# Kernel optimization log

Measured on AMD Instinct MI355X. Metric: run time of the kernel, lower is better.

Reference implementation:

```python
import jax, jax.numpy as jnp
import numpy as np

NP, NA = 60000, 30000          # paper / author node counts
EC, EW, EB = 300000, 150000, 150000
IN_F, HID, H, D, NCLS = 1024, 512, 4, 128, 153  # HID = H*D


def setup_inputs() -> dict:
    key = jax.random.key(0)
    ks = jax.random.split(key, 24)
    inp = {
        "x_paper": jax.random.normal(ks[0], (NP, IN_F), jnp.float32),
        "x_author": jax.random.normal(ks[1], (NA, IN_F), jnp.float32),
        "cites_src": jax.random.randint(ks[2], (EC,), 0, NP, jnp.int32),
        "cites_dst": jax.random.randint(ks[3], (EC,), 0, NP, jnp.int32),
        "writes_src": jax.random.randint(ks[4], (EW,), 0, NA, jnp.int32),
        "writes_dst": jax.random.randint(ks[5], (EW,), 0, NP, jnp.int32),
        "wb_src": jax.random.randint(ks[6], (EB,), 0, NP, jnp.int32),
        "wb_dst": jax.random.randint(ks[7], (EB,), 0, NA, jnp.int32),
        "W0": jax.random.normal(ks[8], (3, IN_F, HID), jnp.float32) * 0.02,
        "al0": jax.random.normal(ks[9], (3, H, D), jnp.float32) * 0.1,
        "ar0": jax.random.normal(ks[10], (3, H, D), jnp.float32) * 0.1,
        "W1": jax.random.normal(ks[11], (3, HID, HID), jnp.float32) * 0.03,
        "al1": jax.random.normal(ks[12], (3, H, D), jnp.float32) * 0.1,
        "ar1": jax.random.normal(ks[13], (3, H, D), jnp.float32) * 0.1,
        "W2": jax.random.normal(ks[14], (3, HID, HID), jnp.float32) * 0.03,
        "al2": jax.random.normal(ks[15], (3, H, D), jnp.float32) * 0.1,
        "ar2": jax.random.normal(ks[16], (3, H, D), jnp.float32) * 0.1,
        "linW": jax.random.normal(ks[17], (HID, NCLS), jnp.float32) * 0.02,
        "linb": jnp.zeros((NCLS,), jnp.float32),
    }
    return inp


def gat_conv(h_src, h_dst, src, dst, W, al, ar, n_dst):
    """DGL-style GATConv on one edge type (bipartite block, shared fc)."""
    zs = (h_src @ W).reshape(-1, H, D)            # (Ns,H,D)
    zd = (h_dst @ W).reshape(-1, H, D)            # (Nd,H,D)
    el = jnp.sum(zs * al, axis=-1)                # (Ns,H)
    er = jnp.sum(zd * ar, axis=-1)                # (Nd,H)
    e = jax.nn.leaky_relu(el[src] + er[dst], 0.2)  # (E,H)
    # edge softmax over incoming edges per destination node
    m = jax.ops.segment_max(e, dst, num_segments=n_dst)
    m = jnp.where(jnp.isfinite(m), m, 0.0)
    ee = jnp.exp(e - m[dst])
    s = jax.ops.segment_sum(ee, dst, num_segments=n_dst)
    a = ee / (s[dst] + 1e-9)                      # (E,H)
    # weighted message aggregation: (Nd,H,D)
    return jax.ops.segment_sum(a[:, :, None] * zs[src], dst, num_segments=n_dst)


def reference(x_paper, x_author, cites_src, cites_dst, writes_src, writes_dst,
              wb_src, wb_dst, W0, al0, ar0, W1, al1, ar1, W2, al2, ar2,
              linW, linb):
    def hetero_layer(hp, ha, W, al, ar, act):
        # HeteroGraphConv: sum-aggregate per destination node type
        op = (gat_conv(hp, hp, cites_src, cites_dst, W[0], al[0], ar[0], NP)
              + gat_conv(ha, hp, writes_src, writes_dst, W[1], al[1], ar[1], NP))
        oa = gat_conv(hp, ha, wb_src, wb_dst, W[2], al[2], ar[2], NA)
        op = op.reshape(NP, H * D)   # head-flatten as in forward()
        oa = oa.reshape(NA, H * D)
        if act:
            op, oa = jax.nn.relu(op), jax.nn.relu(oa)
        return op, oa

    hp, ha = x_paper, x_author
    hp, ha = hetero_layer(hp, ha, W0, al0, ar0, True)
    hp, ha = hetero_layer(hp, ha, W1, al1, ar1, True)
    hp, ha = hetero_layer(hp, ha, W2, al2, ar2, False)  # last layer: no activation
    return hp @ linW + linb
```

## Files before the change

kernel.cpp:

```cpp
#include <hip/hip_runtime.h>
#include <cstddef>
#include <cstdint>

static constexpr int NP = 60000, NA = 30000;
static constexpr int EC = 300000, EW = 150000, EB = 150000;
static constexpr int IN_F = 1024, HID = 512, H = 4, D = 128, NCLS = 153;
static constexpr int MPAD_P = 60160;
static constexpr int MPAD_A = 30208;

typedef __attribute__((ext_vector_type(8))) short short8;
typedef __attribute__((ext_vector_type(4))) float float4v;

__device__ __forceinline__ unsigned short f2bf(float f) {
    unsigned int u = __float_as_uint(f);
    unsigned int r = u + 0x7FFFu + ((u >> 16) & 1u);
    return (unsigned short)(r >> 16);
}
__device__ __forceinline__ float bf2f(unsigned short h) {
    return __uint_as_float(((unsigned int)h) << 16);
}

__device__ __forceinline__ void gll16(const unsigned short* g, unsigned short* l) {
    __builtin_amdgcn_global_load_lds(
        (const __attribute__((address_space(1))) unsigned int*)g,
        (__attribute__((address_space(3))) unsigned int*)l, 16, 0, 0);
}

__global__ void hist_kernel(const int* __restrict__ dst, int E, int* __restrict__ counts) {
    int e = blockIdx.x * 256 + threadIdx.x;
    if (e < E) atomicAdd(&counts[dst[e]], 1);
}

__global__ void exscan_kernel(const int* __restrict__ in, int* __restrict__ out, int n) {
    __shared__ int wsum[4];
    int t = threadIdx.x;
    int lane = t & 63, w = t >> 6;
    int carry = 0;
    const int CH = 256 * 8;
    for (int base = 0; base < n; base += CH) {
        int v[8], run[8];
        int i0 = base + t * 8;
        int tsum = 0;
#pragma unroll
        for (int j = 0; j < 8; ++j) {
            int i = i0 + j;
            v[j] = (i < n) ? in[i] : 0;
            tsum += v[j];
            run[j] = tsum;
        }
        int x = tsum;
#pragma unroll
        for (int off = 1; off < 64; off <<= 1) {
            int y = __shfl_up(x, off);
            if (lane >= off) x += y;
        }
        if (lane == 63) wsum[w] = x;
        __syncthreads();
        int wpre = 0;
        for (int ww = 0; ww < w; ++ww) wpre += wsum[ww];
        int chunktot = wsum[0] + wsum[1] + wsum[2] + wsum[3];
        int pre = carry + wpre + (x - tsum);
#pragma unroll
        for (int j = 0; j < 8; ++j) {
            int i = i0 + j;
            if (i < n) out[i] = pre + run[j] - v[j];
        }
        carry += chunktot;
        __syncthreads();
    }
    if (t == 0) out[n] = carry;
}

__global__ void fill_kernel(const int* __restrict__ src, const int* __restrict__ dst, int E,
                            int* __restrict__ cursor, int* __restrict__ col) {
    int e = blockIdx.x * 256 + threadIdx.x;
    if (e < E) {
        int pos = atomicAdd(&cursor[dst[e]], 1);
        col[pos] = src[e];
    }
}

__global__ void decomp4_kernel(const float4* __restrict__ x, ushort4* __restrict__ hi,
                               ushort4* __restrict__ lo, int M, int K, int Mpad) {
    size_t i4 = (size_t)blockIdx.x * 256 + threadIdx.x;
    size_t tot = ((size_t)Mpad * K) >> 2;
    if (i4 >= tot) return;
    size_t row = (i4 * 4) / (size_t)K;
    float4 v = make_float4(0.f, 0.f, 0.f, 0.f);
    if (row < (size_t)M) v = x[i4];
    ushort4 h, l;
    h.x = f2bf(v.x); h.y = f2bf(v.y); h.z = f2bf(v.z); h.w = f2bf(v.w);
    l.x = f2bf(v.x - bf2f(h.x)); l.y = f2bf(v.y - bf2f(h.y));
    l.z = f2bf(v.z - bf2f(h.z)); l.w = f2bf(v.w - bf2f(h.w));
    hi[i4] = h; lo[i4] = l;
}

__global__ void btprep_kernel(const float* __restrict__ W, unsigned short* __restrict__ hi,
                              unsigned short* __restrict__ lo, int K, int N, int Npad) {
    int i = blockIdx.x * 256 + threadIdx.x;
    if (i >= Npad * K) return;
    int n = i / K, k = i - n * K;
    float v = (n < N) ? W[(size_t)k * N + n] : 0.f;
    unsigned short h = f2bf(v);
    hi[i] = h;
    lo[i] = f2bf(v - bf2f(h));
}

__global__ __launch_bounds__(512, 2) void gemm_6ph(
    const unsigned short* __restrict__ Ahi, const unsigned short* __restrict__ Alo,
    const unsigned short* __restrict__ Bhi, const unsigned short* __restrict__ Blo,
    const float* __restrict__ bias, float* __restrict__ C,
    int M, int K, int Nstore, int ldc) {
    extern __shared__ unsigned short lds[];
    const int tid = threadIdx.x;
    const int lane = tid & 63;
    const int w = tid >> 6;
    const int wr = w >> 2, wc = w & 3;
    const int bm = blockIdx.y * 256, bn = blockIdx.x * 256;

    const int st_row = w * 16 + (lane >> 2);
    const int st_sc = (((lane & 3) ^ ((lane >> 3) & 3)) << 3);
    const size_t aoff0 = (size_t)(bm + st_row) * K + st_sc;
    const size_t aoff1 = aoff0 + (size_t)128 * K;
    const size_t boff0 = (size_t)(bn + st_row) * K + st_sc;
    const size_t boff1 = boff0 + (size_t)128 * K;
    const int ldsAo = w * 512;
    const int ldsBo = 8192 + w * 512;

    const int arow = wr * 128 + (lane & 15);
    const int brow = wc * 64 + (lane & 15);
    const int rq = ((((lane >> 4) & 3) ^ ((lane >> 1) & 3)) << 3);
    const int aRead = arow * 32 + rq;
    const int bRead = 8192 + brow * 32 + rq;

    float4v acc[8][4];
    float4v zf = {0.f, 0.f, 0.f, 0.f};
#pragma unroll
    for (int i = 0; i < 8; ++i)
#pragma unroll
        for (int j = 0; j < 4; ++j) acc[i][j] = zf;

#define WAITV(n) asm volatile("s_waitcnt vmcnt(" #n ")" ::: "memory")
#define BARF()                                 \
    do {                                       \
        asm volatile("" ::: "memory");         \
        __builtin_amdgcn_s_barrier();          \
        asm volatile("" ::: "memory");         \
    } while (0)
#define PRIO1 __builtin_amdgcn_s_setprio(1)
#define PRIO0 __builtin_amdgcn_s_setprio(0)
#define MF(a, b, c) __builtin_amdgcn_mfma_f32_16x16x32_bf16(a, b, c, 0, 0, 0)

#define CHUNK(RG, DOSTAGE, KN, W2STMT, W6STMT)                                        \
    do {                                                                              \
        const unsigned short* sA = &lds[(RG) * 16384u];             \
        const unsigned short* sB = &lds[((RG) + 1u) * 16384u];      \
        unsigned short* dA = &lds[((RG) ^ 2u) * 16384u];                              \
        unsigned short* dB = &lds[(((RG) ^ 2u) + 1u) * 16384u];                       \
        short8 fahi[8], falo[8], fbhi[4], fblo[4];                                    \
                                                                  \
        _Pragma("unroll") for (int i = 0; i < 4; ++i)                                 \
            fahi[i] = *(const short8*)&sA[aRead + i * 512];                           \
        _Pragma("unroll") for (int j = 0; j < 4; ++j)                                 \
            fbhi[j] = *(const short8*)&sA[bRead + j * 512];                           \
        if (DOSTAGE) {                                                                \
            gll16(Ahi + aoff0 + (KN), dA + ldsAo);                                    \
            gll16(Ahi + aoff1 + (KN), dA + ldsAo + 4096);                             \
        }                                                                             \
        BARF(); PRIO1;                                                                \
        _Pragma("unroll") for (int i = 0; i < 4; ++i)                                 \
            _Pragma("unroll") for (int j = 0; j < 4; ++j)                             \
                acc[i][j] = MF(fahi[i], fbhi[j], acc[i][j]);                          \
        PRIO0; BARF();                                                                \
                                                                  \
        _Pragma("unroll") for (int i = 0; i < 4; ++i)                                 \
            fahi[i + 4] = *(const short8*)&sA[aRead + (i + 4) * 512];                 \
        if (DOSTAGE) {                                                                \
            gll16(Bhi + boff0 + (KN), dA + ldsBo);                                    \
            gll16(Bhi + boff1 + (KN), dA + ldsBo + 4096);                             \
        }                                                                             \
        BARF(); PRIO1;                                                                \
        _Pragma("unroll") for (int i = 0; i < 4; ++i)                                 \
            _Pragma("unroll") for (int j = 0; j < 4; ++j)                             \
                acc[i + 4][j] = MF(fahi[i + 4], fbhi[j], acc[i + 4][j]);              \
        PRIO0; W2STMT; BARF();                                                        \
                                                                  \
        _Pragma("unroll") for (int i = 0; i < 4; ++i)                                 \
            falo[i] = *(const short8*)&sB[aRead + i * 512];                           \
        if (DOSTAGE) {                                                                \
            gll16(Alo + aoff0 + (KN), dB + ldsAo);                                    \
            gll16(Alo + aoff1 + (KN), dB + ldsAo + 4096);                             \
        }                                                                             \
        BARF(); PRIO1;                                                                \
        _Pragma("unroll") for (int i = 0; i < 4; ++i)                                 \
            _Pragma("unroll") for (int j = 0; j < 4; ++j)                             \
                acc[i][j] = MF(falo[i], fbhi[j], acc[i][j]);                          \
        PRIO0; BARF();                                                                \
                                                                  \
        _Pragma("unroll") for (int i = 0; i < 4; ++i)                                 \
            falo[i + 4] = *(const short8*)&sB[aRead + (i + 4) * 512];                 \
        if (DOSTAGE) {                                                                \
            gll16(Blo + boff0 + (KN), dB + ldsBo);                                    \
            gll16(Blo + boff1 + (KN), dB + ldsBo + 4096);                             \
        }                                                                             \
        BARF(); PRIO1;                                                                \
        _Pragma("unroll") for (int i = 0; i < 4; ++i)                                 \
            _Pragma("unroll") for (int j = 0; j < 4; ++j)                             \
                acc[i + 4][j] = MF(falo[i + 4], fbhi[j], acc[i + 4][j]);              \
        PRIO0; BARF();                                                                \
                                      \
        _Pragma("unroll") for (int j = 0; j < 4; ++j)                                 \
            fblo[j] = *(const short8*)&sB[bRead + j * 512];                           \
        BARF(); PRIO1;                                                                \
        _Pragma("unroll") for (int i = 0; i < 8; ++i)                                 \
            _Pragma("unroll") for (int j = 0; j < 4; ++j)                             \
                acc[i][j] = MF(fahi[i], fblo[j], acc[i][j]);                          \
        PRIO0; W6STMT; BARF();                                                        \
    } while (0)

    gll16(Ahi + aoff0, &lds[0] + ldsAo);
    gll16(Ahi + aoff1, &lds[0] + ldsAo + 4096);
    gll16(Bhi + boff0, &lds[0] + ldsBo);
    gll16(Bhi + boff1, &lds[0] + ldsBo + 4096);
    gll16(Alo + aoff0, &lds[16384] + ldsAo);
    gll16(Alo + aoff1, &lds[16384] + ldsAo + 4096);
    gll16(Blo + boff0, &lds[16384] + ldsBo);
    gll16(Blo + boff1, &lds[16384] + ldsBo + 4096);
    WAITV(4);
    BARF();

    unsigned rg = 0;
    const int nK = K >> 5;
#pragma unroll 1
    for (int c = 0; c < nK - 1; ++c) {
        const int kn = (c + 1) << 5;
        CHUNK(rg, 1, kn, WAITV(4), WAITV(4));
        rg ^= 2;
    }
    CHUNK(rg, 0, 0, WAITV(0), (void)0);
#undef CHUNK
#undef MF
#undef PRIO1
#undef PRIO0
#undef WAITV
#undef BARF

    const int col0 = bn + wc * 64 + (lane & 15);
    const int row0 = bm + wr * 128 + ((lane >> 4) << 2);
#pragma unroll
    for (int i = 0; i < 8; ++i) {
#pragma unroll
        for (int j = 0; j < 4; ++j) {
            int col = col0 + j * 16;
            if (col >= Nstore) continue;
            float badd = bias ? bias[col] : 0.f;
            int rowb = row0 + i * 16;
#pragma unroll
            for (int k = 0; k < 4; ++k) {
                int row = rowb + k;
                if (row < M) C[(size_t)row * ldc + col] = acc[i][j][k] + badd;
            }
        }
    }
}

__global__ __launch_bounds__(256) void eler_kernel(
    const float* __restrict__ z, const float* __restrict__ al, const float* __restrict__ ar,
    float* __restrict__ el, float* __restrict__ er, int M) {
    int row = blockIdx.x * 4 + (threadIdx.x >> 6);
    int lane = threadIdx.x & 63;
    if (row >= M) return;
    const float4* zr = (const float4*)(z + (size_t)row * 512 + lane * 8);
    float4 z0 = zr[0], z1 = zr[1];
    const float4* alp = (const float4*)(al + lane * 8);
    float4 a0 = alp[0], a1 = alp[1];
    float s = z0.x * a0.x + z0.y * a0.y + z0.z * a0.z + z0.w * a0.w
            + z1.x * a1.x + z1.y * a1.y + z1.z * a1.z + z1.w * a1.w;
    s += __shfl_xor(s, 8); s += __shfl_xor(s, 4); s += __shfl_xor(s, 2); s += __shfl_xor(s, 1);
    int h = lane >> 4;
    if ((lane & 15) == 0) el[(size_t)row * 4 + h] = s;
    if (er) {
        const float4* arp = (const float4*)(ar + lane * 8);
        float4 b0 = arp[0], b1 = arp[1];
        float t = z0.x * b0.x + z0.y * b0.y + z0.z * b0.z + z0.w * b0.w
                + z1.x * b1.x + z1.y * b1.y + z1.z * b1.z + z1.w * b1.w;
        t += __shfl_xor(t, 8); t += __shfl_xor(t, 4); t += __shfl_xor(t, 2); t += __shfl_xor(t, 1);
        if ((lane & 15) == 0) er[(size_t)row * 4 + h] = t;
    }
}

__global__ void fold_kernel(const float* __restrict__ W, const float* __restrict__ ar,
                            float* __restrict__ v, int K) {
    int i = blockIdx.x * 256 + threadIdx.x;
    if (i >= K * 4) return;
    int k = i >> 2, h = i & 3;
    const float* wr = W + (size_t)k * 512 + h * 128;
    const float* a = ar + h * 128;
    float s = 0.f;
#pragma unroll 4
    for (int d = 0; d < 128; ++d) s += wr[d] * a[d];
    v[i] = s;
}

__global__ __launch_bounds__(256) void skinny_kernel(
    const float* __restrict__ h, const float* __restrict__ v,
    float* __restrict__ er, int M, int K) {
    __shared__ float vs[4096];
    for (int i = threadIdx.x; i < K * 4; i += 256) vs[i] = v[i];
    __syncthreads();
    int row = blockIdx.x * 4 + (threadIdx.x >> 6);
    int lane = threadIdx.x & 63;
    if (row >= M) return;
    const float* hr = h + (size_t)row * K;
    float a0 = 0, a1 = 0, a2 = 0, a3 = 0;
    for (int k = lane; k < K; k += 64) {
        float x = hr[k];
        float4 vv = *(const float4*)&vs[k * 4];
        a0 += x * vv.x; a1 += x * vv.y; a2 += x * vv.z; a3 += x * vv.w;
    }
#pragma unroll
    for (int off = 32; off; off >>= 1) {
        a0 += __shfl_xor(a0, off); a1 += __shfl_xor(a1, off);
        a2 += __shfl_xor(a2, off); a3 += __shfl_xor(a3, off);
    }
    if (lane == 0) *(float4*)&er[(size_t)row * 4] = make_float4(a0, a1, a2, a3);
}

__global__ __launch_bounds__(256) void agg_fused(
    const int* __restrict__ rp1, const int* __restrict__ col1, const float* __restrict__ z1,
    const float* __restrict__ el1, const float* __restrict__ er1,
    const int* __restrict__ rp2, const int* __restrict__ col2, const float* __restrict__ z2,
    const float* __restrict__ el2, const float* __restrict__ er2,
    float* __restrict__ out, unsigned short* __restrict__ hi, unsigned short* __restrict__ lo,
    int N, int do_relu) {
    int j = blockIdx.x * 4 + (threadIdx.x >> 6);
    int lane = threadIdx.x & 63;
    if (j >= N) return;
    int h = lane >> 4;
    float4 acc0 = make_float4(0, 0, 0, 0), acc1 = make_float4(0, 0, 0, 0);

    {
        int e0 = rp1[j], e1 = rp1[j + 1];
        float erh = er1[(size_t)j * 4 + h];
        float m = -INFINITY, s = 0.f;
        for (int e = e0; e < e1; ++e) {
            float x = el1[(size_t)col1[e] * 4 + h] + erh;
            x = (x >= 0.f) ? x : 0.2f * x;
            float mn = fmaxf(m, x);
            s = s * expf(m - mn) + expf(x - mn);
            m = mn;
        }
        float inv = 1.0f / (s + 1e-9f);
        for (int e = e0; e < e1; ++e) {
            int src = col1[e];
            float x = el1[(size_t)src * 4 + h] + erh;
            x = (x >= 0.f) ? x : 0.2f * x;
            float wgt = expf(x - m) * inv;
            const float4* zr = (const float4*)(z1 + (size_t)src * 512 + lane * 8);
            float4 za = zr[0], zb = zr[1];
            acc0.x += wgt * za.x; acc0.y += wgt * za.y; acc0.z += wgt * za.z; acc0.w += wgt * za.w;
            acc1.x += wgt * zb.x; acc1.y += wgt * zb.y; acc1.z += wgt * zb.z; acc1.w += wgt * zb.w;
        }
    }
    if (rp2) {
        int e0 = rp2[j], e1 = rp2[j + 1];
        float erh = er2[(size_t)j * 4 + h];
        float m = -INFINITY, s = 0.f;
        for (int e = e0; e < e1; ++e) {
            float x = el2[(size_t)col2[e] * 4 + h] + erh;
            x = (x >= 0.f) ? x : 0.2f * x;
            float mn = fmaxf(m, x);
            s = s * expf(m - mn) + expf(x - mn);
            m = mn;
        }
        float inv = 1.0f / (s + 1e-9f);
        for (int e = e0; e < e1; ++e) {
            int src = col2[e];
            float x = el2[(size_t)src * 4 + h] + erh;
            x = (x >= 0.f) ? x : 0.2f * x;
            float wgt = expf(x - m) * inv;
            const float4* zr = (const float4*)(z2 + (size_t)src * 512 + lane * 8);
            float4 za = zr[0], zb = zr[1];
            acc0.x += wgt * za.x; acc0.y += wgt * za.y; acc0.z += wgt * za.z; acc0.w += wgt * za.w;
            acc1.x += wgt * zb.x; acc1.y += wgt * zb.y; acc1.z += wgt * zb.z; acc1.w += wgt * zb.w;
        }
    }
    if (do_relu) {
        acc0.x = fmaxf(acc0.x, 0.f); acc0.y = fmaxf(acc0.y, 0.f);
        acc0.z = fmaxf(acc0.z, 0.f); acc0.w = fmaxf(acc0.w, 0.f);
        acc1.x = fmaxf(acc1.x, 0.f); acc1.y = fmaxf(acc1.y, 0.f);
        acc1.z = fmaxf(acc1.z, 0.f); acc1.w = fmaxf(acc1.w, 0.f);
    }
    float* op = out + (size_t)j * 512 + lane * 8;
    *(float4*)op = acc0;
    *(float4*)(op + 4) = acc1;
    if (hi) {
        size_t base = (size_t)j * 512 + lane * 8;
        ushort4 h0, h1, l0, l1;
        h0.x = f2bf(acc0.x); h0.y = f2bf(acc0.y); h0.z = f2bf(acc0.z); h0.w = f2bf(acc0.w);
        h1.x = f2bf(acc1.x); h1.y = f2bf(acc1.y); h1.z = f2bf(acc1.z); h1.w = f2bf(acc1.w);
        l0.x = f2bf(acc0.x - bf2f(h0.x)); l0.y = f2bf(acc0.y - bf2f(h0.y));
        l0.z = f2bf(acc0.z - bf2f(h0.z)); l0.w = f2bf(acc0.w - bf2f(h0.w));
        l1.x = f2bf(acc1.x - bf2f(h1.x)); l1.y = f2bf(acc1.y - bf2f(h1.y));
        l1.z = f2bf(acc1.z - bf2f(h1.z)); l1.w = f2bf(acc1.w - bf2f(h1.w));
        *(ushort4*)(hi + base) = h0;
        *(ushort4*)(hi + base + 4) = h1;
        *(ushort4*)(lo + base) = l0;
        *(ushort4*)(lo + base + 4) = l1;
    }
}

extern "C" void kernel_launch(void* const* d_in, const int* in_sizes, int n_in,
                              void* d_out, int out_size, void* d_ws, size_t ws_size,
                              hipStream_t stream) {
    const float* x_paper = (const float*)d_in[0];
    const float* x_author = (const float*)d_in[1];
    const int* cites_src = (const int*)d_in[2];
    const int* cites_dst = (const int*)d_in[3];
    const int* writes_src = (const int*)d_in[4];
    const int* writes_dst = (const int*)d_in[5];
    const int* wb_src = (const int*)d_in[6];
    const int* wb_dst = (const int*)d_in[7];
    const float* W0 = (const float*)d_in[8];
    const float* al0 = (const float*)d_in[9];
    const float* ar0 = (const float*)d_in[10];
    const float* W1 = (const float*)d_in[11];
    const float* al1 = (const float*)d_in[12];
    const float* ar1 = (const float*)d_in[13];
    const float* W2 = (const float*)d_in[14];
    const float* al2 = (const float*)d_in[15];
    const float* ar2 = (const float*)d_in[16];
    const float* linW = (const float*)d_in[17];
    const float* linb = (const float*)d_in[18];
    float* out = (float*)d_out;

    (void)hipFuncSetAttribute((const void*)gemm_6ph,
                              hipFuncAttributeMaxDynamicSharedMemorySize, 131072);

    char* p = (char*)d_ws;
    auto alloc = [&](size_t n) { char* r = p; p += (n + 255) & ~(size_t)255; return r; };

    float* hpA = (float*)alloc((size_t)NP * 512 * 4);
    float* hpB = (float*)alloc((size_t)NP * 512 * 4);
    float* haA = (float*)alloc((size_t)NA * 512 * 4);
    float* haB = (float*)alloc((size_t)NA * 512 * 4);
    float* zbuf = (float*)alloc((size_t)NP * 512 * 4);
    float* elA = (float*)alloc((size_t)NP * 16);
    float* erA = (float*)alloc((size_t)NP * 16);
    float* elB = (float*)alloc((size_t)NP * 16);
    float* erB = (float*)alloc((size_t)NP * 16);
    float* vfold = (float*)alloc(4096 * 4);
    int* rp_c = (int*)alloc((NP + 1) * 4);
    int* col_c = (int*)alloc((size_t)EC * 4);
    int* rp_w = (int*)alloc((NP + 1) * 4);
    int* col_w = (int*)alloc((size_t)EW * 4);
    int* rp_b = (int*)alloc((NA + 1) * 4);
    int* col_b = (int*)alloc((size_t)EB * 4);
    int* cursor = (int*)alloc((NP + 1) * 4);
    int* counts = (int*)alloc((size_t)NP * 4);

    unsigned short* AhiP = (unsigned short*)alloc((size_t)MPAD_P * 1024 * 2);
    unsigned short* AloP = (unsigned short*)alloc((size_t)MPAD_P * 1024 * 2);
    unsigned short* AhiA = (unsigned short*)alloc((size_t)MPAD_A * 1024 * 2);
    unsigned short* AloA = (unsigned short*)alloc((size_t)MPAD_A * 1024 * 2);
    const int Ks[3] = {IN_F, HID, HID};
    unsigned short *bthi[3][3], *btlo[3][3];
    for (int l = 0; l < 3; ++l)
        for (int t = 0; t < 3; ++t) {
            bthi[l][t] = (unsigned short*)alloc((size_t)512 * Ks[l] * 2);
            btlo[l][t] = (unsigned short*)alloc((size_t)512 * Ks[l] * 2);
        }
    unsigned short* btLhi = (unsigned short*)alloc((size_t)256 * 512 * 2);
    unsigned short* btLlo = (unsigned short*)alloc((size_t)256 * 512 * 2);
    (void)ws_size;

    struct EdgeT { const int* src; const int* dst; int E; int n; int* rp; int* col; };
    EdgeT ets[3] = {
        {cites_src, cites_dst, EC, NP, rp_c, col_c},
        {writes_src, writes_dst, EW, NP, rp_w, col_w},
        {wb_src, wb_dst, EB, NA, rp_b, col_b},
    };
    for (int t = 0; t < 3; ++t) {
        hipMemsetAsync(counts, 0, (size_t)ets[t].n * 4, stream);
        hist_kernel<<<(ets[t].E + 255) / 256, 256, 0, stream>>>(ets[t].dst, ets[t].E, counts);
        exscan_kernel<<<1, 256, 0, stream>>>(counts, ets[t].rp, ets[t].n);
        hipMemcpyAsync(cursor, ets[t].rp, (size_t)ets[t].n * 4, hipMemcpyDeviceToDevice, stream);
        fill_kernel<<<(ets[t].E + 255) / 256, 256, 0, stream>>>(ets[t].src, ets[t].dst, ets[t].E, cursor, ets[t].col);
    }

    const float* Wl[3] = {W0, W1, W2};
    const float* alL[3] = {al0, al1, al2};
    const float* arL[3] = {ar0, ar1, ar2};

    for (int l = 0; l < 3; ++l) {
        int K = Ks[l];
        for (int t = 0; t < 3; ++t)
            btprep_kernel<<<(512 * K + 255) / 256, 256, 0, stream>>>(
                Wl[l] + (size_t)t * K * 512, bthi[l][t], btlo[l][t], K, 512, 512);
    }
    btprep_kernel<<<(256 * 512 + 255) / 256, 256, 0, stream>>>(linW, btLhi, btLlo, 512, NCLS, 256);

    decomp4_kernel<<<((size_t)MPAD_P * 1024 / 4 + 255) / 256, 256, 0, stream>>>(
        (const float4*)x_paper, (ushort4*)AhiP, (ushort4*)AloP, NP, 1024, MPAD_P);
    decomp4_kernel<<<((size_t)MPAD_A * 1024 / 4 + 255) / 256, 256, 0, stream>>>(
        (const float4*)x_author, (ushort4*)AhiA, (ushort4*)AloA, NA, 1024, MPAD_A);

    auto gemm = [&](const unsigned short* Ah, const unsigned short* Al,
                    const unsigned short* Bh, const unsigned short* Bl,
                    const float* bias, float* C, int M, int Mpad, int K, int gx,
                    int Nstore, int ldc) {
        dim3 g(gx, Mpad / 256);
        gemm_6ph<<<g, 512, 131072, stream>>>(Ah, Al, Bh, Bl, bias, C, M, K, Nstore, ldc);
    };

    const float* hp = x_paper;
    const float* ha = x_author;
    for (int l = 0; l < 3; ++l) {
        int K = Ks[l];
        float* hp_n = (l & 1) ? hpB : hpA;
        float* ha_n = (l & 1) ? haB : haA;
        float* zbuf_w = ha_n;
        const float* W = Wl[l];
        const float* al = alL[l];
        const float* ar = arL[l];
        size_t wstride = (size_t)K * 512;
        int relu = (l < 2) ? 1 : 0;

        gemm(AhiP, AloP, bthi[l][0], btlo[l][0], nullptr, zbuf, NP, MPAD_P, K, 2, 512, 512);
        gemm(AhiA, AloA, bthi[l][1], btlo[l][1], nullptr, zbuf_w, NA, MPAD_A, K, 2, 512, 512);
        eler_kernel<<<(NP + 3) / 4, 256, 0, stream>>>(zbuf, al, ar, elA, erA, NP);
        eler_kernel<<<(NA + 3) / 4, 256, 0, stream>>>(zbuf_w, al + 512, nullptr, elB, nullptr, NA);
        fold_kernel<<<(K * 4 + 255) / 256, 256, 0, stream>>>(W + wstride, ar + 512, vfold, K);
        skinny_kernel<<<(NP + 3) / 4, 256, 0, stream>>>(hp, vfold, erB, NP, K);
        agg_fused<<<(NP + 3) / 4, 256, 0, stream>>>(
            rp_c, col_c, zbuf, elA, erA,
            rp_w, col_w, zbuf_w, elB, erB,
            hp_n, nullptr, nullptr, NP, relu);
        gemm(AhiP, AloP, bthi[l][2], btlo[l][2], nullptr, zbuf, NP, MPAD_P, K, 2, 512, 512);
        decomp4_kernel<<<((size_t)MPAD_P * 512 / 4 + 255) / 256, 256, 0, stream>>>(
            (const float4*)hp_n, (ushort4*)AhiP, (ushort4*)AloP, NP, 512, MPAD_P);
        eler_kernel<<<(NP + 3) / 4, 256, 0, stream>>>(zbuf, al + 1024, nullptr, elA, nullptr, NP);
        fold_kernel<<<(K * 4 + 255) / 256, 256, 0, stream>>>(W + 2 * wstride, ar + 1024, vfold, K);
        skinny_kernel<<<(NA + 3) / 4, 256, 0, stream>>>(ha, vfold, erA, NA, K);
        agg_fused<<<(NA + 3) / 4, 256, 0, stream>>>(
            rp_b, col_b, zbuf, elA, erA,
            nullptr, nullptr, nullptr, nullptr, nullptr,
            ha_n, (l < 2) ? AhiA : nullptr, (l < 2) ? AloA : nullptr, NA, relu);
        hp = hp_n;
        ha = ha_n;
    }
    gemm(AhiP, AloP, btLhi, btLlo, linb, out, NP, MPAD_P, 512, 1, NCLS, NCLS);
}
```

Measured before the change: 3.216 ms.

## Restructure split-bf16 GEMM chunk into register-prefetched five-phase pipeline

```diff
diff --git a/kernel.cpp b/kernel.cpp
--- a/kernel.cpp
+++ b/kernel.cpp
@@ -106,7 +106,7 @@
     lo[i] = f2bf(v - bf2f(h));
 }
 
-__global__ __launch_bounds__(512, 2) void gemm_6ph(
+__global__ __launch_bounds__(512, 2) void gemm_ra(
     const unsigned short* __restrict__ Ahi, const unsigned short* __restrict__ Alo,
     const unsigned short* __restrict__ Bhi, const unsigned short* __restrict__ Blo,
     const float* __restrict__ bias, float* __restrict__ C,
@@ -140,82 +140,93 @@
 #pragma unroll
         for (int j = 0; j < 4; ++j) acc[i][j] = zf;
 
-#define WAITV(n) asm volatile("s_waitcnt vmcnt(" #n ")" ::: "memory")
-#define BARF()                                 \
-    do {                                       \
-        asm volatile("" ::: "memory");         \
-        __builtin_amdgcn_s_barrier();          \
-        asm volatile("" ::: "memory");         \
+    short8 faL[4], fbL[4], faU[4], flL[4], flU[4], fblo[4], nxA[4], nxB[4];
+
+#define SBAR() __builtin_amdgcn_sched_barrier(0)
+#define WAITV(n)                                      \
+    do {                                              \
+        asm volatile("s_waitcnt vmcnt(" #n ")");      \
+        SBAR();                                       \
+    } while (0)
+#define BAR()                                         \
+    do {                                              \
+        SBAR();                                       \
+        __builtin_amdgcn_s_barrier();                 \
+        SBAR();                                       \
     } while (0)
 #define PRIO1 __builtin_amdgcn_s_setprio(1)
 #define PRIO0 __builtin_amdgcn_s_setprio(0)
 #define MF(a, b, c) __builtin_amdgcn_mfma_f32_16x16x32_bf16(a, b, c, 0, 0, 0)
 
-#define CHUNK(RG, DOSTAGE, KN, W2STMT, W6STMT)                                        \
+#define CHUNK(RG, DOSTAGE, KN, W1STMT, W3STMT, W4STMT, LASTC)                         \
     do {                                                                              \
         const unsigned short* sA = &lds[(RG) * 16384u];             \
         const unsigned short* sB = &lds[((RG) + 1u) * 16384u];      \
         unsigned short* dA = &lds[((RG) ^ 2u) * 16384u];                              \
         unsigned short* dB = &lds[(((RG) ^ 2u) + 1u) * 16384u];                       \
-        short8 fahi[8], falo[8], fbhi[4], fblo[4];                                    \
-                                                                  \
-        _Pragma("unroll") for (int i = 0; i < 4; ++i)                                 \
-            fahi[i] = *(const short8*)&sA[aRead + i * 512];                           \
-        _Pragma("unroll") for (int j = 0; j < 4; ++j)                                 \
-            fbhi[j] = *(const short8*)&sA[bRead + j * 512];                           \
+                            \
+        _Pragma("unroll") for (int i = 0; i < 4; ++i)                                 \
+            faU[i] = *(const short8*)&sA[aRead + (i + 4) * 512];                      \
         if (DOSTAGE) {                                                                \
             gll16(Ahi + aoff0 + (KN), dA + ldsAo);                                    \
             gll16(Ahi + aoff1 + (KN), dA + ldsAo + 4096);                             \
         }                                                                             \
-        BARF(); PRIO1;                                                                \
-        _Pragma("unroll") for (int i = 0; i < 4; ++i)                                 \
-            _Pragma("unroll") for (int j = 0; j < 4; ++j)                             \
-                acc[i][j] = MF(fahi[i], fbhi[j], acc[i][j]);                          \
-        PRIO0; BARF();                                                                \
-                                                                  \
-        _Pragma("unroll") for (int i = 0; i < 4; ++i)                                 \
-            fahi[i + 4] = *(const short8*)&sA[aRead + (i + 4) * 512];                 \
+        PRIO1;                                                                        \
+        _Pragma("unroll") for (int i = 0; i < 4; ++i)                                 \
+            _Pragma("unroll") for (int j = 0; j < 4; ++j)                             \
+                acc[i][j] = MF(faL[i], fbL[j], acc[i][j]);                            \
+        PRIO0; W1STMT; BAR();                                                         \
+                                  \
+        _Pragma("unroll") for (int i = 0; i < 4; ++i)                                 \
+            flL[i] = *(const short8*)&sB[aRead + i * 512];                            \
         if (DOSTAGE) {                                                                \
             gll16(Bhi + boff0 + (KN), dA + ldsBo);                                    \
             gll16(Bhi + boff1 + (KN), dA + ldsBo + 4096);                             \
         }                                                                             \
-        BARF(); PRIO1;                                                                \
-        _Pragma("unroll") for (int i = 0; i < 4; ++i)                                 \
-            _Pragma("unroll") for (int j = 0; j < 4; ++j)                             \
-                acc[i + 4][j] = MF(fahi[i + 4], fbhi[j], acc[i + 4][j]);              \
-        PRIO0; W2STMT; BARF();                                                        \
-                                                                  \
-        _Pragma("unroll") for (int i = 0; i < 4; ++i)                                 \
-            falo[i] = *(const short8*)&sB[aRead + i * 512];                           \
+        PRIO1;                                                                        \
+        _Pragma("unroll") for (int i = 0; i < 4; ++i)                                 \
+            _Pragma("unroll") for (int j = 0; j < 4; ++j)                             \
+                acc[i + 4][j] = MF(faU[i], fbL[j], acc[i + 4][j]);                    \
+        PRIO0; BAR();                                                                 \
+                                 \
+        _Pragma("unroll") for (int i = 0; i < 4; ++i)                                 \
+            flU[i] = *(const short8*)&sB[aRead + (i + 4) * 512];                      \
         if (DOSTAGE) {                                                                \
             gll16(Alo + aoff0 + (KN), dB + ldsAo);                                    \
             gll16(Alo + aoff1 + (KN), dB + ldsAo + 4096);                             \
         }                                                                             \
-        BARF(); PRIO1;                                                                \
-        _Pragma("unroll") for (int i = 0; i < 4; ++i)                                 \
-            _Pragma("unroll") for (int j = 0; j < 4; ++j)                             \
-                acc[i][j] = MF(falo[i], fbhi[j], acc[i][j]);                          \
-        PRIO0; BARF();                                                                \
-                                                                  \
-        _Pragma("unroll") for (int i = 0; i < 4; ++i)                                 \
-            falo[i + 4] = *(const short8*)&sB[aRead + (i + 4) * 512];                 \
+        PRIO1;                                                                        \
+        _Pragma("unroll") for (int i = 0; i < 4; ++i)                                 \
+            _Pragma("unroll") for (int j = 0; j < 4; ++j)                             \
+                acc[i][j] = MF(flL[i], fbL[j], acc[i][j]);                            \
+        PRIO0; W3STMT; BAR();                                                         \
+                                 \
+        _Pragma("unroll") for (int j = 0; j < 4; ++j)                                 \
+            fblo[j] = *(const short8*)&sB[bRead + j * 512];                           \
         if (DOSTAGE) {                                                                \
             gll16(Blo + boff0 + (KN), dB + ldsBo);                                    \
             gll16(Blo + boff1 + (KN), dB + ldsBo + 4096);                             \
         }                                                                             \
-        BARF(); PRIO1;                                                                \
-        _Pragma("unroll") for (int i = 0; i < 4; ++i)                                 \
-            _Pragma("unroll") for (int j = 0; j < 4; ++j)                             \
-                acc[i + 4][j] = MF(falo[i + 4], fbhi[j], acc[i + 4][j]);              \
-        PRIO0; BARF();                                                                \
-                                      \
-        _Pragma("unroll") for (int j = 0; j < 4; ++j)                                 \
-            fblo[j] = *(const short8*)&sB[bRead + j * 512];                           \
-        BARF(); PRIO1;                                                                \
-        _Pragma("unroll") for (int i = 0; i < 8; ++i)                                 \
-            _Pragma("unroll") for (int j = 0; j < 4; ++j)                             \
-                acc[i][j] = MF(fahi[i], fblo[j], acc[i][j]);                          \
-        PRIO0; W6STMT; BARF();                                                        \
+        PRIO1;                                                                        \
+        _Pragma("unroll") for (int i = 0; i < 4; ++i)                                 \
+            _Pragma("unroll") for (int j = 0; j < 4; ++j)                             \
+                acc[i + 4][j] = MF(flU[i], fbL[j], acc[i + 4][j]);                    \
+        PRIO0; W4STMT; BAR();                                                         \
+             \
+        if (!(LASTC)) {                                                               \
+            _Pragma("unroll") for (int i = 0; i < 4; ++i)                             \
+                nxA[i] = *(const short8*)&dA[aRead + i * 512];                        \
+            _Pragma("unroll") for (int j = 0; j < 4; ++j)                             \
+                nxB[j] = *(const short8*)&dA[bRead + j * 512];                        \
+        }                                                                             \
+        PRIO1;                                                                        \
+        _Pragma("unroll") for (int i = 0; i < 4; ++i)                                 \
+            _Pragma("unroll") for (int j = 0; j < 4; ++j)                             \
+                acc[i][j] = MF(faL[i], fblo[j], acc[i][j]);                           \
+        _Pragma("unroll") for (int i = 0; i < 4; ++i)                                 \
+            _Pragma("unroll") for (int j = 0; j < 4; ++j)                             \
+                acc[i + 4][j] = MF(faU[i], fblo[j], acc[i + 4][j]);                   \
+        PRIO0; BAR();                                                                 \
     } while (0)
 
     gll16(Ahi + aoff0, &lds[0] + ldsAo);
@@ -227,23 +238,30 @@
     gll16(Blo + boff0, &lds[16384] + ldsBo);
     gll16(Blo + boff1, &lds[16384] + ldsBo + 4096);
     WAITV(4);
-    BARF();
+    BAR();
+#pragma unroll
+    for (int i = 0; i < 4; ++i) faL[i] = *(const short8*)&lds[aRead + i * 512];
+#pragma unroll
+    for (int j = 0; j < 4; ++j) fbL[j] = *(const short8*)&lds[bRead + j * 512];
 
     unsigned rg = 0;
     const int nK = K >> 5;
 #pragma unroll 1
     for (int c = 0; c < nK - 1; ++c) {
         const int kn = (c + 1) << 5;
-        CHUNK(rg, 1, kn, WAITV(4), WAITV(4));
+        CHUNK(rg, 1, kn, WAITV(4), WAITV(6), WAITV(4), 0);
+#pragma unroll
+        for (int i = 0; i < 4; ++i) { faL[i] = nxA[i]; fbL[i] = nxB[i]; }
         rg ^= 2;
     }
-    CHUNK(rg, 0, 0, WAITV(0), (void)0);
+    CHUNK(rg, 0, 0, WAITV(2), WAITV(0), (void)0, 1);
 #undef CHUNK
 #undef MF
 #undef PRIO1
 #undef PRIO0
+#undef BAR
 #undef WAITV
-#undef BARF
+#undef SBAR
 
     const int col0 = bn + wc * 64 + (lane & 15);
     const int row0 = bm + wr * 128 + ((lane >> 4) << 2);
@@ -434,7 +452,7 @@
     const float* linb = (const float*)d_in[18];
     float* out = (float*)d_out;
 
-    (void)hipFuncSetAttribute((const void*)gemm_6ph,
+    (void)hipFuncSetAttribute((const void*)gemm_ra,
                               hipFuncAttributeMaxDynamicSharedMemorySize, 131072);
 
     char* p = (char*)d_ws;
@@ -510,7 +528,7 @@
                     const float* bias, float* C, int M, int Mpad, int K, int gx,
                     int Nstore, int ldc) {
         dim3 g(gx, Mpad / 256);
-        gemm_6ph<<<g, 512, 131072, stream>>>(Ah, Al, Bh, Bl, bias, C, M, K, Nstore, ldc);
+        gemm_ra<<<g, 512, 131072, stream>>>(Ah, Al, Bh, Bl, bias, C, M, K, Nstore, ldc);
     };
 
     const float* hp = x_paper;
```

Measured after the change: 3.190 ms. About the same (-0.8%).
